# Kernel optimization log

Hardware: AMD Instinct MI355X
Metric: run time of the kernel (lower is better)

## Reference

```python
import jax, jax.numpy as jnp
import numpy as np

B, N, OBJ_D, L, EMB_D, H, NANS, VOCAB = 256, 100, 2048, 14, 300, 1024, 3129, 19901


def gru_last_hidden(x, wih, whh, bih, bhh):
    # x: [B, L, EMB_D]; PyTorch GRU gate order (r, z, n); returns last hidden [B, H]
    h0 = jnp.zeros((x.shape[0], whh.shape[0]), x.dtype)

    def step(h, xt):
        gi = xt @ wih + bih          # [B, 3H]
        gh = h @ whh + bhh           # [B, 3H]
        ir, iz, inn = jnp.split(gi, 3, axis=-1)
        hr, hz, hn = jnp.split(gh, 3, axis=-1)
        r = jax.nn.sigmoid(ir + hr)
        z = jax.nn.sigmoid(iz + hz)
        n = jnp.tanh(inn + r * hn)
        h = (1.0 - z) * n + z * h
        return h, None

    h, _ = jax.lax.scan(step, h0, jnp.swapaxes(x, 0, 1))
    return h


def setup_inputs() -> dict:
    key = jax.random.key(0)
    ks = jax.random.split(key, 24)
    g = lambda k, shp, s: jax.random.normal(k, shp, dtype=jnp.float32) * s
    inp = {
        "v": g(ks[0], (B, N, OBJ_D), 1.0),
        "b": jax.random.uniform(ks[1], (B, N, 6), dtype=jnp.float32),
        "det": jax.random.randint(ks[2], (B, N), 0, 1600),
        "q": jax.random.randint(ks[3], (B, L), 0, VOCAB),
        "labels": jax.random.randint(ks[4], (B,), 0, NANS),
        # word embedding
        "emb": g(ks[5], (VOCAB, EMB_D), 0.02),
        # GRU (input 300 -> hidden 1024)
        "gru_wih": g(ks[6], (EMB_D, 3 * H), 0.02),
        "gru_whh": g(ks[7], (H, 3 * H), 0.02),
        "gru_bih": jnp.zeros((3 * H,), jnp.float32),
        "gru_bhh": jnp.zeros((3 * H,), jnp.float32),
        # q_net FCNet
        "wq_net": g(ks[8], (H, H), 0.02),
        "bq_net": jnp.zeros((H,), jnp.float32),
        # s_rel: spatial relation scorer (uses b[:,:,:4])
        "ws_b": g(ks[9], (4, H), 0.1),
        "ws_q": g(ks[10], (H, H), 0.02),
        # v_rel: visual relation scorer
        "wv_v": g(ks[11], (OBJ_D, H), 0.02),
        "wv_q": g(ks[12], (H, H), 0.02),
        # v_att: NewAttention
        "wa_v": g(ks[13], (OBJ_D, H), 0.02),
        "wa_q": g(ks[14], (H, H), 0.02),
        "wa_out": g(ks[15], (H,), 0.02),
        # v_net FCNet
        "wv_net": g(ks[16], (OBJ_D, H), 0.02),
        "bv_net": jnp.zeros((H,), jnp.float32),
        # classifier MLP 1024 -> 2048 -> 3129
        "wc1": g(ks[17], (H, 2 * H), 0.02),
        "bc1": jnp.zeros((2 * H,), jnp.float32),
        "wc2": g(ks[18], (2 * H, NANS), 0.02),
        "bc2": jnp.zeros((NANS,), jnp.float32),
    }
    return inp


def reference(v, b, det, q, labels, emb, gru_wih, gru_whh, gru_bih, gru_bhh,
              wq_net, bq_net, ws_b, ws_q, wv_v, wv_q, wa_v, wa_q, wa_out,
              wv_net, bv_net, wc1, bc1, wc2, bc2):
    # question encoding
    w_emb = emb[q]                                           # [B, L, 300]
    q_emb = gru_last_hidden(w_emb, gru_wih, gru_whh, gru_bih, gru_bhh)  # [B, H]
    q_repr = jax.nn.relu(q_emb @ wq_net + bq_net)            # [B, H]

    # pairwise relation matrices conditioned on the question
    b4 = b[:, :, :4]                                         # [B, N, 4]
    s_proj = jnp.tanh(b4 @ ws_b)                             # [B, N, H]
    s_q = jnp.tanh(q_emb @ ws_q)                             # [B, H]
    s_rel = jnp.einsum('bnh,bmh->bnm', s_proj * s_q[:, None, :], s_proj)

    v_proj = jnp.tanh(v @ wv_v)                              # [B, N, H]
    v_q = jnp.tanh(q_emb @ wv_q)                             # [B, H]
    v_rel = jnp.einsum('bnh,bmh->bnm', v_proj * v_q[:, None, :], v_proj)

    rel = jax.nn.softmax(s_rel + v_rel, axis=2)              # [B, N, N]
    v_nbr = jnp.einsum('bnm,bmd->bnd', rel, v)               # neighbor aggregation
    v2 = v + v_nbr                                           # [B, N, OBJ_D]

    # attention pooling
    av = jax.nn.relu(v2 @ wa_v)                              # [B, N, H]
    aq = jax.nn.relu(q_emb @ wa_q)                           # [B, H]
    att_logits = (av * aq[:, None, :]) @ wa_out              # [B, N]
    v_att = jax.nn.softmax(att_logits, axis=1)[:, :, None]   # [B, N, 1]
    v_emb = (v_att * v2).sum(axis=1)                         # [B, OBJ_D]

    v_repr = jax.nn.relu(v_emb @ wv_net + bv_net)            # [B, H]
    joint = q_repr * v_repr                                  # [B, H]
    logits = jax.nn.relu(joint @ wc1 + bc1) @ wc2 + bc2      # [B, NANS]
    return logits
```

## Files before the change

kernel.cpp:

```cpp
#include <hip/hip_runtime.h>
#include <math.h>

#define B_    256
#define N_    100
#define OBJD  2048
#define L_    14
#define EMBD  300
#define H_    1024
#define H3    3072
#define NANS_ 3129

typedef unsigned short u16;
typedef unsigned int   u32;
typedef long long      ll;
typedef __attribute__((ext_vector_type(8))) short    s16x8;
typedef __attribute__((ext_vector_type(8))) u16      u16x8;
typedef __attribute__((ext_vector_type(4))) float    f32x4;

__device__ __forceinline__ void split2(float x, u16& h, u16& l) {
    const u32 u = __float_as_uint(x);
    h = (u16)(u >> 16);
    const float r = x - __uint_as_float(u & 0xffff0000u);
    l = (u16)(__float_as_uint(r) >> 16);
}
__device__ __forceinline__ float b2f(u16 v) { return __uint_as_float(((u32)v) << 16); }
__device__ __forceinline__ float tanh_fast(float v) {
    const float e = __expf(2.f * v);
    return 1.f - 2.f * __builtin_amdgcn_rcpf(e + 1.f);
}

template<int BM,int BN,int BK,int TM,int TN,int ACT,int EPI,bool GATHER>
__global__ __launch_bounds__(256)
void gemm_f32(const float* __restrict__ A, long long sA, int lda,
              const float* __restrict__ Bm, long long sB, int ldb,
              const float* __restrict__ bias,
              const float* __restrict__ src, long long sSrc, int ldsrc,
              float* __restrict__ C, u16* __restrict__ Chi, u16* __restrict__ Clo,
              long long sC, int ldc,
              int M, int N, int K, const int* __restrict__ gidx)
{
    static_assert((BM*BK)%1024==0 && (BK*BN)%1024==0 && (BM/TM)*(BN/TN)==256, "cfg");
    constexpr int AV = (BM*BK)/1024, BV = (BK*BN)/1024;
    __shared__ float As[BK][BM+4];
    __shared__ float Bs[BK][BN+4];
    const int bz = blockIdx.z;
    A  += (long long)bz * sA;
    Bm += (long long)bz * sB;
    if (EPI != 3) C += (long long)bz * sC;
    if (EPI) src += (long long)bz * sSrc;
    if constexpr (EPI == 3) { Chi += (long long)bz * sC; Clo += (long long)bz * sC; }

    const int tid = threadIdx.x;
    const int m0 = blockIdx.y * BM, n0 = blockIdx.x * BN;
    const int tx = tid % (BN/TN), ty = tid / (BN/TN);
    const bool bvec = ((ldb & 3) == 0);

    float acc[TM][TN];
#pragma unroll
    for (int i=0;i<TM;i++)
#pragma unroll
      for (int j=0;j<TN;j++) acc[i][j] = 0.f;

    for (int k0 = 0; k0 < K; k0 += BK) {
#pragma unroll
        for (int u=0; u<AV; u++) {
            const int flat = (tid + u*256) * 4;
            const int r = flat / BK, c = flat % BK;
            const int gr = m0 + r, gk = k0 + c;
            float4 a4 = make_float4(0.f,0.f,0.f,0.f);
            if (gr < M) {
                const float* arow = GATHER ? (A + (long long)gidx[gr]*lda)
                                           : (A + (long long)gr*lda);
                if (gk + 3 < K) a4 = *(const float4*)(arow + gk);
                else {
                    float t0[4] = {0.f,0.f,0.f,0.f};
#pragma unroll
                    for (int i=0;i<4;i++) if (gk+i < K) t0[i] = arow[gk+i];
                    a4 = make_float4(t0[0],t0[1],t0[2],t0[3]);
                }
            }
            As[c+0][r]=a4.x; As[c+1][r]=a4.y; As[c+2][r]=a4.z; As[c+3][r]=a4.w;
        }
#pragma unroll
        for (int u=0; u<BV; u++) {
            const int flat = (tid + u*256) * 4;
            const int r = flat / BN, c = flat % BN;
            const int gk = k0 + r, gc = n0 + c;
            float4 b4 = make_float4(0.f,0.f,0.f,0.f);
            if (gk < K) {
                const float* brow = Bm + (long long)gk * ldb;
                if (bvec && (gc + 3 < N)) b4 = *(const float4*)(brow + gc);
                else {
                    float t0[4] = {0.f,0.f,0.f,0.f};
#pragma unroll
                    for (int i=0;i<4;i++) if (gc+i < N) t0[i] = brow[gc+i];
                    b4 = make_float4(t0[0],t0[1],t0[2],t0[3]);
                }
            }
            Bs[r][c+0]=b4.x; Bs[r][c+1]=b4.y; Bs[r][c+2]=b4.z; Bs[r][c+3]=b4.w;
        }
        __syncthreads();
#pragma unroll
        for (int kk=0;kk<BK;kk++) {
            float a[TM], b[TN];
#pragma unroll
            for (int p=0;p<TM/4;p++) {
                float4 t4 = *(const float4*)&As[kk][ty*TM + 4*p];
                a[4*p]=t4.x; a[4*p+1]=t4.y; a[4*p+2]=t4.z; a[4*p+3]=t4.w;
            }
#pragma unroll
            for (int p=0;p<TN/4;p++) {
                float4 t4 = *(const float4*)&Bs[kk][tx*TN + 4*p];
                b[4*p]=t4.x; b[4*p+1]=t4.y; b[4*p+2]=t4.z; b[4*p+3]=t4.w;
            }
#pragma unroll
            for (int i=0;i<TM;i++)
#pragma unroll
                for (int j=0;j<TN;j++) acc[i][j] = fmaf(a[i], b[j], acc[i][j]);
        }
        __syncthreads();
    }
#pragma unroll
    for (int i=0;i<TM;i++) {
        const int r = m0 + ty*TM + i;
        if (r >= M) continue;
#pragma unroll
        for (int j=0;j<TN;j++) {
            const int c = n0 + tx*TN + j;
            if (c >= N) continue;
            float val = acc[i][j];
            if (bias) val += bias[c];
            if (EPI == 1 || EPI == 3) val += src[(long long)r*ldsrc + c];
            if constexpr (EPI == 3) {
                u16 h, l; split2(val, h, l);
                Chi[(long long)r*ldc + c] = h;
                Clo[(long long)r*ldc + c] = l;
            } else {
                C[(long long)r*ldc + c] = val;
            }
        }
    }
}

__global__ __launch_bounds__(256)
void split_transpose_w(const float* __restrict__ W, u16* __restrict__ Thi,
                       u16* __restrict__ Tlo, int Kin, int Nin, int Kld)
{
    __shared__ float tile[64][33];
    const int k0 = blockIdx.x*64, n0 = blockIdx.y*32;
    const int t = threadIdx.x;
    const int ln = t & 31, lk = t >> 5;
#pragma unroll
    for (int i=0;i<8;i++) {
        const int k = k0 + lk + i*8, n = n0 + ln;
        tile[lk + i*8][ln] = (k < Kin && n < Nin) ? W[(long long)k*Nin + n] : 0.f;
    }
    __syncthreads();
    const int wn = t >> 3, wk = (t & 7) * 8;
    u16x8 hv, lv;
#pragma unroll
    for (int i=0;i<8;i++){
        u16 h, l; split2(tile[wk + i][wn], h, l);
        hv[i] = h; lv[i] = l;
    }
    *(u16x8*)&Thi[(long long)(n0+wn)*Kld + k0 + wk] = hv;
    *(u16x8*)&Tlo[(long long)(n0+wn)*Kld + k0 + wk] = lv;
}

__global__ __launch_bounds__(256)
void split_rows(const float* __restrict__ x, u16* __restrict__ hi,
                u16* __restrict__ lo, long long n8)
{
    for (long long i = blockIdx.x*256 + threadIdx.x; i < n8; i += (long long)gridDim.x*256) {
        const float4 a = ((const float4*)x)[2*i];
        const float4 c = ((const float4*)x)[2*i+1];
        const float f[8] = {a.x,a.y,a.z,a.w,c.x,c.y,c.z,c.w};
        u16x8 h, l;
#pragma unroll
        for (int e=0;e<8;e++){ u16 hh,ll_; split2(f[e],hh,ll_); h[e]=hh; l[e]=ll_; }
        ((u16x8*)hi)[i] = h;
        ((u16x8*)lo)[i] = l;
    }
}

template<int BM, int ACT, int EPI, bool BIAS>
__global__ __launch_bounds__(256, (BM==256)?2:3)
void gemm3s(const u16* __restrict__ Ahi, const u16* __restrict__ Alo, int lda,
            const u16* __restrict__ BThi, const u16* __restrict__ BTlo,
            const float* __restrict__ bias,
            const float* __restrict__ src, int ldsrc,
            float* __restrict__ C, u16* __restrict__ Chi, u16* __restrict__ Clo,
            int ldc, int N, int K)
{
    constexpr int BN=128, BK=32, PK=40;
    constexpr int MF = BM/32;
    __shared__ __align__(16) u16 smem[2*BM*PK + 2*BN*PK];
    u16* Ah = smem;
    u16* Al = smem + BM*PK;
    u16* Bh = smem + 2*BM*PK;
    u16* Bl = Bh + BN*PK;

    const int tid = threadIdx.x;
    const int m0 = blockIdx.y*BM, n0 = blockIdx.x*BN;
    const int wave = tid>>6, lane = tid&63;
    const int wm = wave>>1, wn = wave&1;
    const int r16 = lane&15, g = lane>>4;

    f32x4 acc[MF][4];
#pragma unroll
    for (int i=0;i<MF;i++)
#pragma unroll
      for (int j=0;j<4;j++) acc[i][j] = f32x4{0.f,0.f,0.f,0.f};

    const int ar = (BM==256) ? tid : (tid>>2);
    const int ac = (BM==256) ? 0   : ((tid&3)*8);
    const u16* pAh = Ahi + (long long)(m0+ar)*lda + ac;
    const u16* pAl = Alo + (long long)(m0+ar)*lda + ac;
    u16* sAh = Ah + ar*PK + ac;
    u16* sAl = Al + ar*PK + ac;
    const int br = tid>>1, bc = (tid&1)*16;
    const u16* pBh = BThi + (long long)(n0+br)*K + bc;
    const u16* pBl = BTlo + (long long)(n0+br)*K + bc;
    u16* sBh = Bh + br*PK + bc;
    u16* sBl = Bl + br*PK + bc;

    for (int k0=0; k0<K; k0+=BK) {
        __syncthreads();
        if constexpr (BM==256) {
#pragma unroll
            for (int u=0;u<4;u++){
                *(u16x8*)(sAh+u*8) = *(const u16x8*)(pAh + k0 + u*8);
                *(u16x8*)(sAl+u*8) = *(const u16x8*)(pAl + k0 + u*8);
            }
        } else {
            *(u16x8*)sAh = *(const u16x8*)(pAh + k0);
            *(u16x8*)sAl = *(const u16x8*)(pAl + k0);
        }
        *(u16x8*)(sBh)   = *(const u16x8*)(pBh + k0);
        *(u16x8*)(sBh+8) = *(const u16x8*)(pBh + k0 + 8);
        *(u16x8*)(sBl)   = *(const u16x8*)(pBl + k0);
        *(u16x8*)(sBl+8) = *(const u16x8*)(pBl + k0 + 8);
        __syncthreads();

        s16x8 bh[4], bl[4];
#pragma unroll
        for (int nf=0;nf<4;nf++){
            bh[nf] = *(const s16x8*)&Bh[(wn*64 + nf*16 + r16)*PK + g*8];
            bl[nf] = *(const s16x8*)&Bl[(wn*64 + nf*16 + r16)*PK + g*8];
        }
#pragma unroll
        for (int mf=0; mf<MF; mf++){
            const s16x8 ah = *(const s16x8*)&Ah[(wm*(BM/2) + mf*16 + r16)*PK + g*8];
            const s16x8 al = *(const s16x8*)&Al[(wm*(BM/2) + mf*16 + r16)*PK + g*8];
#pragma unroll
            for (int nf=0;nf<4;nf++){
                acc[mf][nf] = __builtin_amdgcn_mfma_f32_16x16x32_bf16(ah, bh[nf], acc[mf][nf], 0,0,0);
                acc[mf][nf] = __builtin_amdgcn_mfma_f32_16x16x32_bf16(ah, bl[nf], acc[mf][nf], 0,0,0);
                acc[mf][nf] = __builtin_amdgcn_mfma_f32_16x16x32_bf16(al, bh[nf], acc[mf][nf], 0,0,0);
            }
        }
    }
#pragma unroll
    for (int mf=0;mf<MF;mf++){
        const int rr = m0 + wm*(BM/2) + mf*16 + g*4;
#pragma unroll
        for (int nf=0;nf<4;nf++){
            const int cc = n0 + wn*64 + nf*16 + r16;
            if (cc >= N) continue;
            const float bval = BIAS ? bias[cc] : 0.f;
#pragma unroll
            for (int i=0;i<4;i++){
                float val = acc[mf][nf][i] + bval;
                if (ACT == 1) val = fmaxf(val, 0.f);
                else if (ACT == 2) val = tanh_fast(val);
                else if (ACT == 3) {
                    const int seg = cc >> 10;
                    val = (seg==0 || seg==3) ? fmaxf(val, 0.f) : tanh_fast(val);
                }
                if (EPI == 2) val *= src[(long long)(rr+i)*ldsrc + cc];
                const long long o = (long long)(rr+i)*ldc + cc;
                C[o] = val;
                if (EPI >= 1) {
                    u16 h, l; split2(val, h, l);
                    Chi[o] = h; Clo[o] = l;
                }
            }
        }
    }
}

__global__ __launch_bounds__(192)
void gru_step(const float* __restrict__ hprev,
              const u16* __restrict__ hHi, const u16* __restrict__ hLo,
              const u16* __restrict__ whhThi, const u16* __restrict__ whhTlo,
              const float* __restrict__ gi, int t, const float* __restrict__ bhh,
              float* __restrict__ hout, u16* __restrict__ hoHi, u16* __restrict__ hoLo)
{
    constexpr int PK = 40;
    __shared__ __align__(16) u16 smem[8*32*PK];
    u16* Ah = smem;
    u16* Al = smem + 32*PK;
    const int tid = threadIdx.x, seg = tid>>6, lane = tid&63;
    u16* Bh = smem + 2*32*PK + seg*2*32*PK;
    u16* Bl = Bh + 32*PK;
    const int j0 = blockIdx.x*32, b0 = blockIdx.y*32;
    const int r16 = lane&15, g = lane>>4;
    f32x4 acc[2][2];
#pragma unroll
    for (int i=0;i<2;i++)
#pragma unroll
      for (int j=0;j<2;j++) acc[i][j] = f32x4{0.f,0.f,0.f,0.f};

    const int sr = lane>>1, sc = (lane&1)*16;
    const u16* pAh = hHi + (long long)(b0+sr)*H_ + sc;
    const u16* pAl = hLo + (long long)(b0+sr)*H_ + sc;
    const u16* pBh = whhThi + (long long)(seg*H_ + j0 + sr)*H_ + sc;
    const u16* pBl = whhTlo + (long long)(seg*H_ + j0 + sr)*H_ + sc;
    u16* sAh = Ah + sr*PK + sc;
    u16* sAl = Al + sr*PK + sc;
    u16* sBh = Bh + sr*PK + sc;
    u16* sBl = Bl + sr*PK + sc;

    for (int k0=0; k0<H_; k0+=32) {
        __syncthreads();
        if (seg == 0) {
            *(u16x8*)(sAh)   = *(const u16x8*)(pAh + k0);
            *(u16x8*)(sAh+8) = *(const u16x8*)(pAh + k0 + 8);
            *(u16x8*)(sAl)   = *(const u16x8*)(pAl + k0);
            *(u16x8*)(sAl+8) = *(const u16x8*)(pAl + k0 + 8);
        }
        *(u16x8*)(sBh)   = *(const u16x8*)(pBh + k0);
        *(u16x8*)(sBh+8) = *(const u16x8*)(pBh + k0 + 8);
        *(u16x8*)(sBl)   = *(const u16x8*)(pBl + k0);
        *(u16x8*)(sBl+8) = *(const u16x8*)(pBl + k0 + 8);
        __syncthreads();
        s16x8 bh[2], bl[2];
#pragma unroll
        for (int nf=0;nf<2;nf++){
            bh[nf] = *(const s16x8*)&Bh[(nf*16 + r16)*PK + g*8];
            bl[nf] = *(const s16x8*)&Bl[(nf*16 + r16)*PK + g*8];
        }
#pragma unroll
        for (int mf=0;mf<2;mf++){
            const s16x8 ah = *(const s16x8*)&Ah[(mf*16 + r16)*PK + g*8];
            const s16x8 al = *(const s16x8*)&Al[(mf*16 + r16)*PK + g*8];
#pragma unroll
            for (int nf=0;nf<2;nf++){
                acc[mf][nf] = __builtin_amdgcn_mfma_f32_16x16x32_bf16(ah, bh[nf], acc[mf][nf], 0,0,0);
                acc[mf][nf] = __builtin_amdgcn_mfma_f32_16x16x32_bf16(ah, bl[nf], acc[mf][nf], 0,0,0);
                acc[mf][nf] = __builtin_amdgcn_mfma_f32_16x16x32_bf16(al, bh[nf], acc[mf][nf], 0,0,0);
            }
        }
    }
    __syncthreads();
    float* ghb = (float*)smem;
#pragma unroll
    for (int mf=0;mf<2;mf++)
#pragma unroll
      for (int nf=0;nf<2;nf++)
#pragma unroll
        for (int i=0;i<4;i++)
            ghb[(seg*32 + mf*16 + g*4 + i)*32 + nf*16 + r16] = acc[mf][nf][i];
    __syncthreads();
    for (int idx = tid; idx < 1024; idx += 192) {
        const int r = idx>>5, c = idx&31;
        const int b = b0 + r, j = j0 + c;
        const float* gib = gi + ((long long)b*L_ + t)*H3 + j;
        const float ir = gib[0], iz = gib[H_], inn = gib[2*H_];
        const float hr = ghb[(0*32+r)*32+c] + bhh[j];
        const float hz = ghb[(1*32+r)*32+c] + bhh[j+H_];
        const float hn = ghb[(2*32+r)*32+c] + bhh[j+2*H_];
        const float hp = hprev[(long long)b*H_ + j];
        const float rg = 1.f/(1.f+expf(-(ir+hr)));
        const float zg = 1.f/(1.f+expf(-(iz+hz)));
        const float nn = tanhf(inn + rg*hn);
        const float ho = (1.f - zg)*nn + zg*hp;
        hout[(long long)b*H_ + j] = ho;
        u16 hh, hl; split2(ho, hh, hl);
        hoHi[(long long)b*H_ + j] = hh;
        hoLo[(long long)b*H_ + j] = hl;
    }
}

__global__ __launch_bounds__(256)
void gru_t0(const float* __restrict__ gi, const float* __restrict__ bhh,
            float* __restrict__ h, u16* __restrict__ hHi, u16* __restrict__ hLo)
{
    const int idx = blockIdx.x*256 + threadIdx.x;
    const int b = idx >> 10, j = idx & (H_-1);
    const float* gib = gi + ((long long)b*L_)*H3 + j;
    const float ir = gib[0], iz = gib[H_], inn = gib[2*H_];
    const float rg = 1.f/(1.f+expf(-(ir+bhh[j])));
    const float zg = 1.f/(1.f+expf(-(iz+bhh[j+H_])));
    const float nn = tanhf(inn + rg*bhh[j+2*H_]);
    const float ho = (1.f - zg)*nn;
    h[idx] = ho;
    u16 hh, hl; split2(ho, hh, hl);
    hHi[idx] = hh; hLo[idx] = hl;
}

__global__ __launch_bounds__(256)
void build_qbias(const float* __restrict__ bq, float* __restrict__ qb)
{
    const int i = blockIdx.x*256 + threadIdx.x;
    if (i < 4096) qb[i] = (i < 1024) ? bq[i] : 0.f;
}

__global__ __launch_bounds__(256)
void sproj_kernel(const float* __restrict__ bIn, const float* __restrict__ wsB,
                  float* __restrict__ sProj)
{
    const int row = blockIdx.x;
    const float* br = bIn + (long long)row * 6;
    const float b0=br[0], b1=br[1], b2=br[2], b3=br[3];
    for (int h = threadIdx.x; h < H_; h += 256) {
        float val = b0*wsB[h] + b1*wsB[H_+h] + b2*wsB[2*H_+h] + b3*wsB[3*H_+h];
        sProj[(long long)row*H_ + h] = tanhf(val);
    }
}

__global__ __launch_bounds__(256)
void gram_rel_kernel(const float* __restrict__ sProj, const float* __restrict__ sQ,
                     const float* __restrict__ vProj, const float* __restrict__ vQ,
                     int ldq, float* __restrict__ rel)
{
    __shared__ float As[16][68];
    __shared__ float Bs[16][68];
    const int b = blockIdx.z;
    const int n0 = blockIdx.y * 64, m0 = blockIdx.x * 64;
    const int tid = threadIdx.x;
    const int lr = tid / 4, lk = (tid % 4) * 4;
    const int tx = tid % 16, ty = tid / 16;
    float acc[4][4];
#pragma unroll
    for (int i=0;i<4;i++)
#pragma unroll
      for (int j=0;j<4;j++) acc[i][j]=0.f;

    for (int pass=0; pass<2; ++pass) {
        const float* P  = pass ? vProj : sProj;
        const float* Q  = (pass ? vQ : sQ) + (long long)b * ldq;
        const float* Pb = P + (long long)b * N_ * H_;
        for (int k0=0; k0<H_; k0+=16) {
            const float4 qv = *(const float4*)(Q + k0 + lk);
            float4 a4 = make_float4(0,0,0,0), b4 = make_float4(0,0,0,0);
            if (n0 + lr < N_) a4 = *(const float4*)(Pb + (long long)(n0+lr)*H_ + k0 + lk);
            if (m0 + lr < N_) b4 = *(const float4*)(Pb + (long long)(m0+lr)*H_ + k0 + lk);
            As[lk+0][lr]=a4.x*qv.x; As[lk+1][lr]=a4.y*qv.y; As[lk+2][lr]=a4.z*qv.z; As[lk+3][lr]=a4.w*qv.w;
            Bs[lk+0][lr]=b4.x; Bs[lk+1][lr]=b4.y; Bs[lk+2][lr]=b4.z; Bs[lk+3][lr]=b4.w;
            __syncthreads();
#pragma unroll
// ... 28 lines not shown
    float* r = rel + ((long long)blockIdx.x*4 + w)*N_;
    const float v0 = r[l];
    const float v1 = (l + 64 < N_) ? r[l+64] : -INFINITY;
    float mx = fmaxf(v0, v1);
    for (int s=32;s;s>>=1) mx = fmaxf(mx, __shfl_xor(mx, s));
    const float e0 = expf(v0-mx);
    const float e1 = (l+64<N_) ? expf(v1-mx) : 0.f;
    float sum = e0+e1;
    for (int s=32;s;s>>=1) sum += __shfl_xor(sum, s);
    const float inv = 1.f/sum;
    r[l] = e0*inv;
    if (l+64 < N_) r[l+64] = e1*inv;
}

__global__ __launch_bounds__(256)
void att_logits_kernel(const float* __restrict__ av, const float* __restrict__ aq,
                       int ldq, const float* __restrict__ waOut, float* __restrict__ out)
{
    const int w = threadIdx.x >> 6, l = threadIdx.x & 63;
    const int row = blockIdx.x*4 + w;
    const int b = row / N_;
    const float* avr = av + (long long)row*H_;
    const float* aqr = aq + (long long)b*ldq;
    float acc = 0.f;
#pragma unroll
    for (int i=0;i<4;i++){
        const int h = i*256 + l*4;
        const float4 a4 = *(const float4*)(avr+h);
        const float4 q4 = *(const float4*)(aqr+h);
        const float4 w4 = *(const float4*)(waOut+h);
        acc += a4.x*q4.x*w4.x + a4.y*q4.y*w4.y + a4.z*q4.z*w4.z + a4.w*q4.w*w4.w;
    }
    for (int s=32;s;s>>=1) acc += __shfl_xor(acc, s);
    if (l==0) out[row] = acc;
}

__global__ __launch_bounds__(128)
void softmax_n_kernel(const float* __restrict__ lg, float* __restrict__ att)
{
    __shared__ float s[128];
    const int b = blockIdx.x, t = threadIdx.x;
    const float v = (t < N_) ? lg[(long long)b*N_+t] : -INFINITY;
    s[t]=v; __syncthreads();
    for (int st=64;st;st>>=1){ if (t<st) s[t]=fmaxf(s[t],s[t+st]); __syncthreads(); }
    const float mx = s[0]; __syncthreads();
    const float e = (t<N_)? expf(v-mx) : 0.f;
    s[t]=e; __syncthreads();
    for (int st=64;st;st>>=1){ if (t<st) s[t]+=s[t+st]; __syncthreads(); }
    const float inv = 1.f/s[0];
    if (t<N_) att[(long long)b*N_+t] = e*inv;
}

__global__ __launch_bounds__(256)
void vemb_kernel(const float* __restrict__ att, const u16* __restrict__ v2hi,
                 const u16* __restrict__ v2lo, u16* __restrict__ veHi,
                 u16* __restrict__ veLo)
{
    __shared__ float sa[N_];
    const int b = blockIdx.y, dt = blockIdx.x, tid = threadIdx.x;
    if (tid < N_) sa[tid] = att[(long long)b*N_+tid];
    __syncthreads();
    const int d = dt*256 + tid;
    const long long base = (long long)b*N_*OBJD + d;
    float acc = 0.f;
#pragma unroll 4
    for (int n=0;n<N_;n++) {
        const long long o = base + (long long)n*OBJD;
        acc += sa[n]*(b2f(v2hi[o]) + b2f(v2lo[o]));
    }
    u16 h, l; split2(acc, h, l);
    veHi[(long long)b*OBJD + d] = h;
    veLo[(long long)b*OBJD + d] = l;
}

extern "C" void kernel_launch(void* const* d_in, const int* in_sizes, int n_in,
                              void* d_out, int out_size, void* d_ws, size_t ws_size,
                              hipStream_t stream)
{
    const float* v      = (const float*)d_in[0];
    const float* bbox   = (const float*)d_in[1];
    const int*   q      = (const int*)  d_in[3];
    const float* emb    = (const float*)d_in[5];
    const float* wih    = (const float*)d_in[6];
    const float* whh    = (const float*)d_in[7];
    const float* bih    = (const float*)d_in[8];
    const float* bhh    = (const float*)d_in[9];
    const float* wq_net = (const float*)d_in[10];
    const float* bq_net = (const float*)d_in[11];
    const float* ws_b   = (const float*)d_in[12];
    const float* ws_q   = (const float*)d_in[13];
    const float* wv_v   = (const float*)d_in[14];
    const float* wv_q   = (const float*)d_in[15];
    const float* wa_v   = (const float*)d_in[16];
    const float* wa_q   = (const float*)d_in[17];
    const float* wa_out = (const float*)d_in[18];
    const float* wv_net = (const float*)d_in[19];
    const float* bv_net = (const float*)d_in[20];
    const float* wc1    = (const float*)d_in[21];
    const float* bc1    = (const float*)d_in[22];
    const float* wc2    = (const float*)d_in[23];
    const float* bc2    = (const float*)d_in[24];
    float* out = (float*)d_out;
    (void)in_sizes; (void)n_in; (void)out_size; (void)ws_size; (void)bih;

    float* ws = (float*)d_ws;
    size_t off = 0;
    auto alloc = [&](size_t n){ float* p = ws + off; off += (n + 63) & ~(size_t)63; return p; };
    float* gi    = alloc((size_t)B_*L_*H3);
    float* h_a   = alloc((size_t)B_*H_);
    float* h_b   = alloc((size_t)B_*H_);
    u16* hhi_a = (u16*)alloc((size_t)B_*H_/2);
    u16* hlo_a = (u16*)alloc((size_t)B_*H_/2);
    u16* hhi_b = (u16*)alloc((size_t)B_*H_/2);
    u16* hlo_b = (u16*)alloc((size_t)B_*H_/2);
    float* qcat  = alloc((size_t)B_*4096);
    float* qbias = alloc(4096);
    float* sproj = alloc((size_t)B_*N_*H_);
    float* vproj = alloc((size_t)B_*N_*H_);
    float* relb  = alloc((size_t)B_*N_*N_);
    u16* vhi = (u16*)alloc((size_t)B_*N_*OBJD/2);
    u16* vlo = (u16*)alloc((size_t)B_*N_*OBJD/2);
    float* avb   = sproj;
    float* attl  = alloc((size_t)B_*N_);
    float* vatt  = alloc((size_t)B_*N_);
    u16* vembHi = (u16*)alloc((size_t)B_*OBJD/2);
    u16* vembLo = (u16*)alloc((size_t)B_*OBJD/2);
    float* jointf = alloc((size_t)B_*H_);
    u16* jointHi = (u16*)alloc((size_t)B_*H_/2);
    u16* jointLo = (u16*)alloc((size_t)B_*H_/2);
    float* c1f   = alloc((size_t)B_*2*H_);
    u16* c1Hi = (u16*)alloc((size_t)B_*H_);
    u16* c1Lo = (u16*)alloc((size_t)B_*H_);
    u16* whhThi = (u16*)alloc((size_t)H3*H_/2);
    u16* whhTlo = (u16*)alloc((size_t)H3*H_/2);
    u16* qcThi  = (u16*)alloc((size_t)4096*H_/2);
    u16* qcTlo  = (u16*)alloc((size_t)4096*H_/2);
    u16* wvvThi = (u16*)alloc((size_t)H_*OBJD/2);
    u16* wvvTlo = (u16*)alloc((size_t)H_*OBJD/2);
    u16* wavThi = (u16*)alloc((size_t)H_*OBJD/2);
    u16* wavTlo = (u16*)alloc((size_t)H_*OBJD/2);
    u16* wvnThi = (u16*)alloc((size_t)H_*OBJD/2);
    u16* wvnTlo = (u16*)alloc((size_t)H_*OBJD/2);
    u16* wc1Thi = (u16*)alloc((size_t)2*H_*H_/2);
    u16* wc1Tlo = (u16*)alloc((size_t)2*H_*H_/2);
    u16* wc2Thi = (u16*)alloc((size_t)3200*2*H_/2);
    u16* wc2Tlo = (u16*)alloc((size_t)3200*2*H_/2);

    split_transpose_w<<<dim3(H_/64, H3/32),256,0,stream>>>(whh, whhThi, whhTlo, H_, H3, H_);
    split_transpose_w<<<dim3(H_/64, H_/32),256,0,stream>>>(wq_net, qcThi + (size_t)0*H_*H_, qcTlo + (size_t)0*H_*H_, H_, H_, H_);
    split_transpose_w<<<dim3(H_/64, H_/32),256,0,stream>>>(ws_q,   qcThi + (size_t)1*H_*H_, qcTlo + (size_t)1*H_*H_, H_, H_, H_);
    split_transpose_w<<<dim3(H_/64, H_/32),256,0,stream>>>(wv_q,   qcThi + (size_t)2*H_*H_, qcTlo + (size_t)2*H_*H_, H_, H_, H_);
    split_transpose_w<<<dim3(H_/64, H_/32),256,0,stream>>>(wa_q,   qcThi + (size_t)3*H_*H_, qcTlo + (size_t)3*H_*H_, H_, H_, H_);
    split_transpose_w<<<dim3(OBJD/64, H_/32),256,0,stream>>>(wv_v, wvvThi, wvvTlo, OBJD, H_, OBJD);
    split_transpose_w<<<dim3(OBJD/64, H_/32),256,0,stream>>>(wa_v, wavThi, wavTlo, OBJD, H_, OBJD);
    split_transpose_w<<<dim3(OBJD/64, H_/32),256,0,stream>>>(wv_net, wvnThi, wvnTlo, OBJD, H_, OBJD);
    split_transpose_w<<<dim3(H_/64, 2*H_/32),256,0,stream>>>(wc1, wc1Thi, wc1Tlo, H_, 2*H_, H_);
    split_transpose_w<<<dim3(2*H_/64, 3200/32),256,0,stream>>>(wc2, wc2Thi, wc2Tlo, 2*H_, NANS_, 2*H_);
    split_rows<<<2048,256,0,stream>>>(v, vhi, vlo, (long long)B_*N_*OBJD/8);
    build_qbias<<<16,256,0,stream>>>(bq_net, qbias);

    {
        dim3 g(H3/128, (B_*L_+127)/128, 1);
        gemm_f32<128,128,16,8,8,0,0,true><<<g,256,0,stream>>>(
            emb,0,EMBD, wih,0,H3, bih, nullptr,0,0, gi,nullptr,nullptr,0,H3, B_*L_, H3, EMBD, q);
    }
    gru_t0<<<(B_*H_)/256,256,0,stream>>>(gi, bhh, h_a, hhi_a, hlo_a);
    float* hp = h_a; u16* hpHi = hhi_a; u16* hpLo = hlo_a;
    float* hn = h_b; u16* hnHi = hhi_b; u16* hnLo = hlo_b;
    for (int t=1;t<L_;t++){
        gru_step<<<dim3(H_/32, B_/32),192,0,stream>>>(hp, hpHi, hpLo, whhThi, whhTlo,
                                                      gi, t, bhh, hn, hnHi, hnLo);
        float* tf=hp; hp=hn; hn=tf;
        u16* th=hpHi; hpHi=hnHi; hnHi=th;
        u16* tl=hpLo; hpLo=hnLo; hnLo=tl;
    }
    gemm3s<64,3,0,true><<<dim3(4096/128, B_/64),256,0,stream>>>(
        hpHi, hpLo, H_, qcThi, qcTlo, qbias, nullptr,0,
        qcat, nullptr, nullptr, 4096, 4096, H_);
    const float* qrepr = qcat;
    const float* sq    = qcat + 1024;
    const float* vq    = qcat + 2048;
    const float* aq    = qcat + 3072;

    sproj_kernel<<<B_*N_,256,0,stream>>>(bbox, ws_b, sproj);
    gemm3s<256,2,0,false><<<dim3(H_/128, (B_*N_)/256),256,0,stream>>>(
        vhi, vlo, OBJD, wvvThi, wvvTlo, nullptr, nullptr,0,
        vproj, nullptr, nullptr, H_, H_, OBJD);
    gram_rel_kernel<<<dim3(2,2,B_),256,0,stream>>>(sproj, sq, vproj, vq, 4096, relb);
    softmax_m_kernel<<<(B_*N_)/4,256,0,stream>>>(relb);
    {
        dim3 g(OBJD/64, (N_+63)/64, B_);
        gemm_f32<64,64,16,4,4,0,3,false><<<g,256,0,stream>>>(
            relb,(long long)N_*N_,N_, v,(long long)N_*OBJD,OBJD, nullptr,
            v,(long long)N_*OBJD,OBJD, nullptr, vhi, vlo,
            (long long)N_*OBJD, OBJD, N_, OBJD, N_, nullptr);
    }
    gemm3s<256,1,0,false><<<dim3(H_/128, (B_*N_)/256),256,0,stream>>>(
        vhi, vlo, OBJD, wavThi, wavTlo, nullptr, nullptr,0,
        avb, nullptr, nullptr, H_, H_, OBJD);
    att_logits_kernel<<<(B_*N_)/4,256,0,stream>>>(avb, aq, 4096, wa_out, attl);
    softmax_n_kernel<<<B_,128,0,stream>>>(attl, vatt);
    vemb_kernel<<<dim3(OBJD/256,B_),256,0,stream>>>(vatt, vhi, vlo, vembHi, vembLo);
    gemm3s<64,1,2,true><<<dim3(H_/128, B_/64),256,0,stream>>>(
        vembHi, vembLo, OBJD, wvnThi, wvnTlo, bv_net, qrepr, 4096,
        jointf, jointHi, jointLo, H_, H_, OBJD);
    gemm3s<64,1,1,true><<<dim3(2*H_/128, B_/64),256,0,stream>>>(
        jointHi, jointLo, H_, wc1Thi, wc1Tlo, bc1, nullptr,0,
        c1f, c1Hi, c1Lo, 2*H_, 2*H_, H_);
    gemm3s<64,0,0,true><<<dim3(3200/128, B_/64),256,0,stream>>>(
        c1Hi, c1Lo, 2*H_, wc2Thi, wc2Tlo, bc2, nullptr,0,
        out, nullptr, nullptr, NANS_, NANS_, 2*H_);
}
```

Before: 2.986 ms.

## Interleave hi/lo bf16 splits per 32-column chunk and retile big GEMMs

Activation hi/lo bf16 halves are now stored interleaved in 32-element chunks within one buffer, so each K-step load fetches both halves from one contiguous 128-byte region. The large v-projection GEMMs move from 256-row tiles to a 128x128 kernel with register prefetch of the next K tile and an XCD-aware block-to-tile mapping meant to improve L2 reuse of A rows. The small GEMMs get a dedicated 64-row kernel with the new layout. The risks are lower occupancy from the extra prefetch registers and more scattered 16-bit stores in the epilogues that write the split.

```diff
diff --git a/kernel.cpp b/kernel.cpp
--- a/kernel.cpp
+++ b/kernel.cpp
@@ -12,7 +12,6 @@
 
 typedef unsigned short u16;
 typedef unsigned int   u32;
-typedef long long      ll;
 typedef __attribute__((ext_vector_type(8))) short    s16x8;
 typedef __attribute__((ext_vector_type(8))) u16      u16x8;
 typedef __attribute__((ext_vector_type(4))) float    f32x4;
@@ -29,13 +28,13 @@
     return 1.f - 2.f * __builtin_amdgcn_rcpf(e + 1.f);
 }
 
-template<int BM,int BN,int BK,int TM,int TN,int ACT,int EPI,bool GATHER>
+template<int BM,int BN,int BK,int TM,int TN,int EPI,bool GATHER>
 __global__ __launch_bounds__(256)
 void gemm_f32(const float* __restrict__ A, long long sA, int lda,
               const float* __restrict__ Bm, long long sB, int ldb,
               const float* __restrict__ bias,
               const float* __restrict__ src, long long sSrc, int ldsrc,
-              float* __restrict__ C, u16* __restrict__ Chi, u16* __restrict__ Clo,
+              float* __restrict__ C, u16* __restrict__ Csp,
               long long sC, int ldc,
               int M, int N, int K, const int* __restrict__ gidx)
 {
@@ -48,7 +47,7 @@
     Bm += (long long)bz * sB;
     if (EPI != 3) C += (long long)bz * sC;
     if (EPI) src += (long long)bz * sSrc;
-    if constexpr (EPI == 3) { Chi += (long long)bz * sC; Clo += (long long)bz * sC; }
+    if constexpr (EPI == 3) Csp += (long long)bz * sC * 2;
 
     const int tid = threadIdx.x;
     const int m0 = blockIdx.y * BM, n0 = blockIdx.x * BN;
@@ -130,11 +129,11 @@
             if (c >= N) continue;
             float val = acc[i][j];
             if (bias) val += bias[c];
-            if (EPI == 1 || EPI == 3) val += src[(long long)r*ldsrc + c];
+            if (EPI == 3) val += src[(long long)r*ldsrc + c];
             if constexpr (EPI == 3) {
                 u16 h, l; split2(val, h, l);
-                Chi[(long long)r*ldc + c] = h;
-                Clo[(long long)r*ldc + c] = l;
+                const long long os = (long long)r*2*ldc + ((c>>5)<<6) + (c&31);
+                Csp[os] = h; Csp[os+32] = l;
             } else {
                 C[(long long)r*ldc + c] = val;
             }
@@ -168,101 +167,179 @@
 }
 
 __global__ __launch_bounds__(256)
-void split_rows(const float* __restrict__ x, u16* __restrict__ hi,
-                u16* __restrict__ lo, long long n8)
-{
-    for (long long i = blockIdx.x*256 + threadIdx.x; i < n8; i += (long long)gridDim.x*256) {
-        const float4 a = ((const float4*)x)[2*i];
-        const float4 c = ((const float4*)x)[2*i+1];
-        const float f[8] = {a.x,a.y,a.z,a.w,c.x,c.y,c.z,c.w};
-        u16x8 h, l;
-#pragma unroll
-        for (int e=0;e<8;e++){ u16 hh,ll_; split2(f[e],hh,ll_); h[e]=hh; l[e]=ll_; }
-        ((u16x8*)hi)[i] = h;
-        ((u16x8*)lo)[i] = l;
-    }
-}
-
-template<int BM, int ACT, int EPI, bool BIAS>
-__global__ __launch_bounds__(256, (BM==256)?2:3)
-void gemm3s(const u16* __restrict__ Ahi, const u16* __restrict__ Alo, int lda,
-            const u16* __restrict__ BThi, const u16* __restrict__ BTlo,
-            const float* __restrict__ bias,
-            const float* __restrict__ src, int ldsrc,
-            float* __restrict__ C, u16* __restrict__ Chi, u16* __restrict__ Clo,
-            int ldc, int N, int K)
-{
-    constexpr int BN=128, BK=32, PK=40;
-    constexpr int MF = BM/32;
-    __shared__ __align__(16) u16 smem[2*BM*PK + 2*BN*PK];
-    u16* Ah = smem;
-    u16* Al = smem + BM*PK;
-    u16* Bh = smem + 2*BM*PK;
-    u16* Bl = Bh + BN*PK;
+void split_rows_il(const float* __restrict__ x, u16* __restrict__ sp, long long ngran)
+{
+    for (long long g = blockIdx.x*256 + threadIdx.x; g < ngran; g += (long long)gridDim.x*256) {
+        const float4* s4 = (const float4*)(x + g*32);
+        u16* o = sp + g*64;
+        u16x8 hv[4], lv[4];
+#pragma unroll
+        for (int q=0;q<4;q++){
+            const float4 f0 = s4[2*q], f1 = s4[2*q+1];
+            const float fa[8]={f0.x,f0.y,f0.z,f0.w,f1.x,f1.y,f1.z,f1.w};
+#pragma unroll
+            for (int e=0;e<8;e++){ u16 hh,ll2; split2(fa[e],hh,ll2); hv[q][e]=hh; lv[q][e]=ll2; }
+        }
+#pragma unroll
+        for (int q=0;q<4;q++){ *(u16x8*)(o+q*8)=hv[q]; *(u16x8*)(o+32+q*8)=lv[q]; }
+    }
+}
+
+template<int ACT>
+__global__ __launch_bounds__(256, 3)
+void gemm3s128(const u16* __restrict__ Asp, int lda2,
+               const u16* __restrict__ BThi, const u16* __restrict__ BTlo,
+               float* __restrict__ C, int ldc, int N, int K, int rpx)
+{
+    constexpr int PK=40;
+    __shared__ __align__(16) u16 Ah[128*PK];
+    __shared__ __align__(16) u16 Al[128*PK];
+    __shared__ __align__(16) u16 Bh[128*PK];
+    __shared__ __align__(16) u16 Bl[128*PK];
+
+    const int wgid = blockIdx.x;
+    const int xcd  = wgid & 7;
+    const int j    = wgid >> 3;
+    const int m0   = (xcd*rpx + (j>>3)) * 128;
+    const int n0   = (j & 7) * 128;
 
     const int tid = threadIdx.x;
-    const int m0 = blockIdx.y*BM, n0 = blockIdx.x*BN;
     const int wave = tid>>6, lane = tid&63;
     const int wm = wave>>1, wn = wave&1;
     const int r16 = lane&15, g = lane>>4;
 
-    f32x4 acc[MF][4];
-#pragma unroll
-    for (int i=0;i<MF;i++)
-#pragma unroll
-      for (int j=0;j<4;j++) acc[i][j] = f32x4{0.f,0.f,0.f,0.f};
-
-    const int ar = (BM==256) ? tid : (tid>>2);
-    const int ac = (BM==256) ? 0   : ((tid&3)*8);
-    const u16* pAh = Ahi + (long long)(m0+ar)*lda + ac;
-    const u16* pAl = Alo + (long long)(m0+ar)*lda + ac;
-    u16* sAh = Ah + ar*PK + ac;
-    u16* sAl = Al + ar*PK + ac;
-    const int br = tid>>1, bc = (tid&1)*16;
-    const u16* pBh = BThi + (long long)(n0+br)*K + bc;
-    const u16* pBl = BTlo + (long long)(n0+br)*K + bc;
-    u16* sBh = Bh + br*PK + bc;
-    u16* sBl = Bl + br*PK + bc;
-
-    for (int k0=0; k0<K; k0+=BK) {
+    f32x4 acc[4][4];
+#pragma unroll
+    for (int i=0;i<4;i++)
+#pragma unroll
+      for (int jj=0;jj<4;jj++) acc[i][jj] = f32x4{0.f,0.f,0.f,0.f};
+
+    const int r = tid>>1, half = tid&1;
+    const u16* pA = Asp + (long long)(m0+r)*lda2 + half*32;
+    const u16* pB = (half ? BTlo : BThi) + (long long)(n0+r)*K;
+    u16* sA = (half ? Al : Ah) + r*PK;
+    u16* sB = (half ? Bl : Bh) + r*PK;
+
+    u16x8 ra0,ra1,ra2,ra3, rb0,rb1,rb2,rb3;
+    {
+        ra0=*(const u16x8*)pA;      ra1=*(const u16x8*)(pA+8);
+        ra2=*(const u16x8*)(pA+16); ra3=*(const u16x8*)(pA+24);
+        rb0=*(const u16x8*)pB;      rb1=*(const u16x8*)(pB+8);
+        rb2=*(const u16x8*)(pB+16); rb3=*(const u16x8*)(pB+24);
+    }
+    for (int k0=0; k0<K; k0+=32) {
         __syncthreads();
-        if constexpr (BM==256) {
-#pragma unroll
-            for (int u=0;u<4;u++){
-                *(u16x8*)(sAh+u*8) = *(const u16x8*)(pAh + k0 + u*8);
-                *(u16x8*)(sAl+u*8) = *(const u16x8*)(pAl + k0 + u*8);
-            }
-        } else {
-            *(u16x8*)sAh = *(const u16x8*)(pAh + k0);
-            *(u16x8*)sAl = *(const u16x8*)(pAl + k0);
-        }
-        *(u16x8*)(sBh)   = *(const u16x8*)(pBh + k0);
-        *(u16x8*)(sBh+8) = *(const u16x8*)(pBh + k0 + 8);
-        *(u16x8*)(sBl)   = *(const u16x8*)(pBl + k0);
-        *(u16x8*)(sBl+8) = *(const u16x8*)(pBl + k0 + 8);
+        *(u16x8*)(sA)=ra0; *(u16x8*)(sA+8)=ra1; *(u16x8*)(sA+16)=ra2; *(u16x8*)(sA+24)=ra3;
+        *(u16x8*)(sB)=rb0; *(u16x8*)(sB+8)=rb1; *(u16x8*)(sB+16)=rb2; *(u16x8*)(sB+24)=rb3;
+        if (k0+32 < K) {
+            const u16* a = pA + (long long)(k0+32)*2;
+            const u16* b = pB + (k0+32);
+            ra0=*(const u16x8*)a;      ra1=*(const u16x8*)(a+8);
+            ra2=*(const u16x8*)(a+16); ra3=*(const u16x8*)(a+24);
+            rb0=*(const u16x8*)b;      rb1=*(const u16x8*)(b+8);
+            rb2=*(const u16x8*)(b+16); rb3=*(const u16x8*)(b+24);
+        }
         __syncthreads();
-
-        s16x8 bh[4], bl[4];
+        s16x8 bhf[4], blf[4];
 #pragma unroll
         for (int nf=0;nf<4;nf++){
-            bh[nf] = *(const s16x8*)&Bh[(wn*64 + nf*16 + r16)*PK + g*8];
-            bl[nf] = *(const s16x8*)&Bl[(wn*64 + nf*16 + r16)*PK + g*8];
-        }
-#pragma unroll
-        for (int mf=0; mf<MF; mf++){
-            const s16x8 ah = *(const s16x8*)&Ah[(wm*(BM/2) + mf*16 + r16)*PK + g*8];
-            const s16x8 al = *(const s16x8*)&Al[(wm*(BM/2) + mf*16 + r16)*PK + g*8];
+            bhf[nf] = *(const s16x8*)&Bh[(wn*64 + nf*16 + r16)*PK + g*8];
+            blf[nf] = *(const s16x8*)&Bl[(wn*64 + nf*16 + r16)*PK + g*8];
+        }
+#pragma unroll
+        for (int mf=0;mf<4;mf++){
+            const s16x8 ah = *(const s16x8*)&Ah[(wm*64 + mf*16 + r16)*PK + g*8];
+            const s16x8 al = *(const s16x8*)&Al[(wm*64 + mf*16 + r16)*PK + g*8];
 #pragma unroll
             for (int nf=0;nf<4;nf++){
-                acc[mf][nf] = __builtin_amdgcn_mfma_f32_16x16x32_bf16(ah, bh[nf], acc[mf][nf], 0,0,0);
-                acc[mf][nf] = __builtin_amdgcn_mfma_f32_16x16x32_bf16(ah, bl[nf], acc[mf][nf], 0,0,0);
-                acc[mf][nf] = __builtin_amdgcn_mfma_f32_16x16x32_bf16(al, bh[nf], acc[mf][nf], 0,0,0);
-            }
-        }
-    }
-#pragma unroll
-    for (int mf=0;mf<MF;mf++){
-        const int rr = m0 + wm*(BM/2) + mf*16 + g*4;
+                acc[mf][nf] = __builtin_amdgcn_mfma_f32_16x16x32_bf16(ah, bhf[nf], acc[mf][nf],0,0,0);
+                acc[mf][nf] = __builtin_amdgcn_mfma_f32_16x16x32_bf16(ah, blf[nf], acc[mf][nf],0,0,0);
+                acc[mf][nf] = __builtin_amdgcn_mfma_f32_16x16x32_bf16(al, bhf[nf], acc[mf][nf],0,0,0);
+            }
+        }
+    }
+#pragma unroll
+    for (int mf=0;mf<4;mf++){
+        const int rr = m0 + wm*64 + mf*16 + g*4;
+#pragma unroll
+        for (int nf=0;nf<4;nf++){
+            const int cc = n0 + wn*64 + nf*16 + r16;
+            if (cc >= N) continue;
+#pragma unroll
+            for (int i=0;i<4;i++){
+                float val = acc[mf][nf][i];
+                if (ACT==1) val = fmaxf(val,0.f);
+                else if (ACT==2) val = tanh_fast(val);
+                C[(long long)(rr+i)*ldc + cc] = val;
+            }
+        }
+    }
+}
+
+template<int ACT, int EPI, bool BIAS>
+__global__ __launch_bounds__(256, 3)
+void gemm3s64(const u16* __restrict__ Asp, int lda2,
+              const u16* __restrict__ BThi, const u16* __restrict__ BTlo,
+              const float* __restrict__ bias,
+              const float* __restrict__ src, int ldsrc,
+              float* __restrict__ C, u16* __restrict__ Csp,
+              int ldc, int N, int K)
+{
+    constexpr int PK=40;
+    __shared__ __align__(16) u16 Ah[64*PK];
+    __shared__ __align__(16) u16 Al[64*PK];
+    __shared__ __align__(16) u16 Bh[128*PK];
+    __shared__ __align__(16) u16 Bl[128*PK];
+
+    const int tid = threadIdx.x;
+    const int m0 = blockIdx.y*64, n0 = blockIdx.x*128;
+    const int wave = tid>>6, lane = tid&63;
+    const int wm = wave>>1, wn = wave&1;
+    const int r16 = lane&15, g = lane>>4;
+
+    f32x4 acc[2][4];
+#pragma unroll
+    for (int i=0;i<2;i++)
+#pragma unroll
+      for (int jj=0;jj<4;jj++) acc[i][jj] = f32x4{0.f,0.f,0.f,0.f};
+
+    const int ar = tid>>2, aq = tid&3;
+    const u16* pA = Asp + (long long)(m0+ar)*lda2 + aq*16;
+    u16* sA = ((aq<2) ? Ah : Al) + ar*PK + (aq&1)*16;
+    const int rb = tid>>1, hb = tid&1;
+    const u16* pB = (hb ? BTlo : BThi) + (long long)(n0+rb)*K;
+    u16* sB = (hb ? Bl : Bh) + rb*PK;
+
+    for (int k0=0; k0<K; k0+=32) {
+        __syncthreads();
+        *(u16x8*)(sA)   = *(const u16x8*)(pA + (long long)k0*2);
+        *(u16x8*)(sA+8) = *(const u16x8*)(pA + (long long)k0*2 + 8);
+        *(u16x8*)(sB)    = *(const u16x8*)(pB + k0);
+        *(u16x8*)(sB+8)  = *(const u16x8*)(pB + k0 + 8);
+        *(u16x8*)(sB+16) = *(const u16x8*)(pB + k0 + 16);
+        *(u16x8*)(sB+24) = *(const u16x8*)(pB + k0 + 24);
+        __syncthreads();
+        s16x8 bhf[4], blf[4];
+#pragma unroll
+        for (int nf=0;nf<4;nf++){
+            bhf[nf] = *(const s16x8*)&Bh[(wn*64 + nf*16 + r16)*PK + g*8];
+            blf[nf] = *(const s16x8*)&Bl[(wn*64 + nf*16 + r16)*PK + g*8];
+        }
+#pragma unroll
+        for (int mf=0;mf<2;mf++){
+            const s16x8 ah = *(const s16x8*)&Ah[(wm*32 + mf*16 + r16)*PK + g*8];
+            const s16x8 al = *(const s16x8*)&Al[(wm*32 + mf*16 + r16)*PK + g*8];
+#pragma unroll
+            for (int nf=0;nf<4;nf++){
+                acc[mf][nf] = __builtin_amdgcn_mfma_f32_16x16x32_bf16(ah, bhf[nf], acc[mf][nf],0,0,0);
+                acc[mf][nf] = __builtin_amdgcn_mfma_f32_16x16x32_bf16(ah, blf[nf], acc[mf][nf],0,0,0);
+                acc[mf][nf] = __builtin_amdgcn_mfma_f32_16x16x32_bf16(al, bhf[nf], acc[mf][nf],0,0,0);
+            }
+        }
+    }
+#pragma unroll
+    for (int mf=0;mf<2;mf++){
+        const int rr = m0 + wm*32 + mf*16 + g*4;
 #pragma unroll
         for (int nf=0;nf<4;nf++){
             const int cc = n0 + wn*64 + nf*16 + r16;
@@ -278,11 +355,11 @@
                     val = (seg==0 || seg==3) ? fmaxf(val, 0.f) : tanh_fast(val);
                 }
                 if (EPI == 2) val *= src[(long long)(rr+i)*ldsrc + cc];
-                const long long o = (long long)(rr+i)*ldc + cc;
-                C[o] = val;
+                C[(long long)(rr+i)*ldc + cc] = val;
                 if (EPI >= 1) {
                     u16 h, l; split2(val, h, l);
-                    Chi[o] = h; Clo[o] = l;
+                    const long long os = (long long)(rr+i)*2*ldc + ((cc>>5)<<6) + (cc&31);
+                    Csp[os] = h; Csp[os+32] = l;
                 }
             }
         }
@@ -290,11 +367,10 @@
 }
 
 __global__ __launch_bounds__(192)
-void gru_step(const float* __restrict__ hprev,
-              const u16* __restrict__ hHi, const u16* __restrict__ hLo,
+void gru_step(const float* __restrict__ hprev, const u16* __restrict__ hsp,
               const u16* __restrict__ whhThi, const u16* __restrict__ whhTlo,
               const float* __restrict__ gi, int t, const float* __restrict__ bhh,
-              float* __restrict__ hout, u16* __restrict__ hoHi, u16* __restrict__ hoLo)
+              float* __restrict__ hout, u16* __restrict__ hosp)
 {
     constexpr int PK = 40;
     __shared__ __align__(16) u16 smem[8*32*PK];
@@ -311,23 +387,23 @@
 #pragma unroll
       for (int j=0;j<2;j++) acc[i][j] = f32x4{0.f,0.f,0.f,0.f};
 
+    const int rA = lane>>1, hA = lane&1;
+    const u16* pA = hsp + (long long)(b0+rA)*(2*H_) + hA*32;
+    u16* sA = (hA ? Al : Ah) + rA*PK;
     const int sr = lane>>1, sc = (lane&1)*16;
-    const u16* pAh = hHi + (long long)(b0+sr)*H_ + sc;
-    const u16* pAl = hLo + (long long)(b0+sr)*H_ + sc;
     const u16* pBh = whhThi + (long long)(seg*H_ + j0 + sr)*H_ + sc;
     const u16* pBl = whhTlo + (long long)(seg*H_ + j0 + sr)*H_ + sc;
-    u16* sAh = Ah + sr*PK + sc;
-    u16* sAl = Al + sr*PK + sc;
     u16* sBh = Bh + sr*PK + sc;
     u16* sBl = Bl + sr*PK + sc;
 
     for (int k0=0; k0<H_; k0+=32) {
         __syncthreads();
         if (seg == 0) {
-            *(u16x8*)(sAh)   = *(const u16x8*)(pAh + k0);
-            *(u16x8*)(sAh+8) = *(const u16x8*)(pAh + k0 + 8);
-            *(u16x8*)(sAl)   = *(const u16x8*)(pAl + k0);
-            *(u16x8*)(sAl+8) = *(const u16x8*)(pAl + k0 + 8);
+            const u16* a = pA + (long long)k0*2;
+            *(u16x8*)(sA)    = *(const u16x8*)(a);
+            *(u16x8*)(sA+8)  = *(const u16x8*)(a+8);
+            *(u16x8*)(sA+16) = *(const u16x8*)(a+16);
+            *(u16x8*)(sA+24) = *(const u16x8*)(a+24);
         }
         *(u16x8*)(sBh)   = *(const u16x8*)(pBh + k0);
         *(u16x8*)(sBh+8) = *(const u16x8*)(pBh + k0 + 8);
@@ -377,14 +453,14 @@
         const float ho = (1.f - zg)*nn + zg*hp;
         hout[(long long)b*H_ + j] = ho;
         u16 hh, hl; split2(ho, hh, hl);
-        hoHi[(long long)b*H_ + j] = hh;
-        hoLo[(long long)b*H_ + j] = hl;
+        const long long ob = (long long)b*(2*H_) + ((j>>5)<<6) + (j&31);
+        hosp[ob] = hh; hosp[ob+32] = hl;
     }
 }
 
 __global__ __launch_bounds__(256)
 void gru_t0(const float* __restrict__ gi, const float* __restrict__ bhh,
-            float* __restrict__ h, u16* __restrict__ hHi, u16* __restrict__ hLo)
+            float* __restrict__ h, u16* __restrict__ hsp)
 {
     const int idx = blockIdx.x*256 + threadIdx.x;
     const int b = idx >> 10, j = idx & (H_-1);
@@ -396,7 +472,8 @@
     const float ho = (1.f - zg)*nn;
     h[idx] = ho;
     u16 hh, hl; split2(ho, hh, hl);
-    hHi[idx] = hh; hLo[idx] = hl;
+    const long long ob = (long long)b*(2*H_) + ((j>>5)<<6) + (j&31);
+    hsp[ob] = hh; hsp[ob+32] = hl;
 }
 
 __global__ __launch_bounds__(256)
@@ -531,25 +608,25 @@
 }
 
 __global__ __launch_bounds__(256)
-void vemb_kernel(const float* __restrict__ att, const u16* __restrict__ v2hi,
-                 const u16* __restrict__ v2lo, u16* __restrict__ veHi,
-                 u16* __restrict__ veLo)
+void vemb_kernel(const float* __restrict__ att, const u16* __restrict__ v2sp,
+                 u16* __restrict__ vesp)
 {
     __shared__ float sa[N_];
     const int b = blockIdx.y, dt = blockIdx.x, tid = threadIdx.x;
     if (tid < N_) sa[tid] = att[(long long)b*N_+tid];
     __syncthreads();
     const int d = dt*256 + tid;
-    const long long base = (long long)b*N_*OBJD + d;
+    const long long colo = (long long)((d>>5)<<6) + (d&31);
+    const u16* vb = v2sp + (long long)b*N_*(2*OBJD) + colo;
     float acc = 0.f;
 #pragma unroll 4
     for (int n=0;n<N_;n++) {
-        const long long o = base + (long long)n*OBJD;
-        acc += sa[n]*(b2f(v2hi[o]) + b2f(v2lo[o]));
+        const u16* p = vb + (long long)n*(2*OBJD);
+        acc += sa[n]*(b2f(p[0]) + b2f(p[32]));
     }
     u16 h, l; split2(acc, h, l);
-    veHi[(long long)b*OBJD + d] = h;
-    veLo[(long long)b*OBJD + d] = l;
+    const long long o = (long long)b*(2*OBJD) + colo;
+    vesp[o] = h; vesp[o+32] = l;
 }
 
 extern "C" void kernel_launch(void* const* d_in, const int* in_sizes, int n_in,
@@ -588,28 +665,22 @@
     float* gi    = alloc((size_t)B_*L_*H3);
     float* h_a   = alloc((size_t)B_*H_);
     float* h_b   = alloc((size_t)B_*H_);
-    u16* hhi_a = (u16*)alloc((size_t)B_*H_/2);
-    u16* hlo_a = (u16*)alloc((size_t)B_*H_/2);
-    u16* hhi_b = (u16*)alloc((size_t)B_*H_/2);
-    u16* hlo_b = (u16*)alloc((size_t)B_*H_/2);
+    u16* hsp_a = (u16*)alloc((size_t)B_*H_);
+    u16* hsp_b = (u16*)alloc((size_t)B_*H_);
     float* qcat  = alloc((size_t)B_*4096);
     float* qbias = alloc(4096);
     float* sproj = alloc((size_t)B_*N_*H_);
     float* vproj = alloc((size_t)B_*N_*H_);
     float* relb  = alloc((size_t)B_*N_*N_);
-    u16* vhi = (u16*)alloc((size_t)B_*N_*OBJD/2);
-    u16* vlo = (u16*)alloc((size_t)B_*N_*OBJD/2);
+    u16* vsp  = (u16*)alloc((size_t)B_*N_*OBJD);
     float* avb   = sproj;
     float* attl  = alloc((size_t)B_*N_);
     float* vatt  = alloc((size_t)B_*N_);
-    u16* vembHi = (u16*)alloc((size_t)B_*OBJD/2);
-    u16* vembLo = (u16*)alloc((size_t)B_*OBJD/2);
+    u16* vembsp = (u16*)alloc((size_t)B_*OBJD);
     float* jointf = alloc((size_t)B_*H_);
-    u16* jointHi = (u16*)alloc((size_t)B_*H_/2);
-    u16* jointLo = (u16*)alloc((size_t)B_*H_/2);
+    u16* jointsp = (u16*)alloc((size_t)B_*H_);
     float* c1f   = alloc((size_t)B_*2*H_);
-    u16* c1Hi = (u16*)alloc((size_t)B_*H_);
-    u16* c1Lo = (u16*)alloc((size_t)B_*H_);
+    u16* c1sp = (u16*)alloc((size_t)B_*2*H_);
     u16* whhThi = (u16*)alloc((size_t)H3*H_/2);
     u16* whhTlo = (u16*)alloc((size_t)H3*H_/2);
     u16* qcThi  = (u16*)alloc((size_t)4096*H_/2);
@@ -635,58 +706,55 @@
     split_transpose_w<<<dim3(OBJD/64, H_/32),256,0,stream>>>(wv_net, wvnThi, wvnTlo, OBJD, H_, OBJD);
     split_transpose_w<<<dim3(H_/64, 2*H_/32),256,0,stream>>>(wc1, wc1Thi, wc1Tlo, H_, 2*H_, H_);
     split_transpose_w<<<dim3(2*H_/64, 3200/32),256,0,stream>>>(wc2, wc2Thi, wc2Tlo, 2*H_, NANS_, 2*H_);
-    split_rows<<<2048,256,0,stream>>>(v, vhi, vlo, (long long)B_*N_*OBJD/8);
+    split_rows_il<<<2048,256,0,stream>>>(v, vsp, (long long)B_*N_*OBJD/32);
     build_qbias<<<16,256,0,stream>>>(bq_net, qbias);
 
     {
         dim3 g(H3/128, (B_*L_+127)/128, 1);
-        gemm_f32<128,128,16,8,8,0,0,true><<<g,256,0,stream>>>(
-            emb,0,EMBD, wih,0,H3, bih, nullptr,0,0, gi,nullptr,nullptr,0,H3, B_*L_, H3, EMBD, q);
-    }
-    gru_t0<<<(B_*H_)/256,256,0,stream>>>(gi, bhh, h_a, hhi_a, hlo_a);
-    float* hp = h_a; u16* hpHi = hhi_a; u16* hpLo = hlo_a;
-    float* hn = h_b; u16* hnHi = hhi_b; u16* hnLo = hlo_b;
+        gemm_f32<128,128,16,8,8,0,true><<<g,256,0,stream>>>(
+            emb,0,EMBD, wih,0,H3, bih, nullptr,0,0, gi,nullptr,0,H3, B_*L_, H3, EMBD, q);
+    }
+    gru_t0<<<(B_*H_)/256,256,0,stream>>>(gi, bhh, h_a, hsp_a);
+    float* hp = h_a; u16* hpS = hsp_a;
+    float* hn = h_b; u16* hnS = hsp_b;
     for (int t=1;t<L_;t++){
-        gru_step<<<dim3(H_/32, B_/32),192,0,stream>>>(hp, hpHi, hpLo, whhThi, whhTlo,
-                                                      gi, t, bhh, hn, hnHi, hnLo);
+        gru_step<<<dim3(H_/32, B_/32),192,0,stream>>>(hp, hpS, whhThi, whhTlo,
+                                                      gi, t, bhh, hn, hnS);
         float* tf=hp; hp=hn; hn=tf;
-        u16* th=hpHi; hpHi=hnHi; hnHi=th;
-        u16* tl=hpLo; hpLo=hnLo; hnLo=tl;
-    }
-    gemm3s<64,3,0,true><<<dim3(4096/128, B_/64),256,0,stream>>>(
-        hpHi, hpLo, H_, qcThi, qcTlo, qbias, nullptr,0,
-        qcat, nullptr, nullptr, 4096, 4096, H_);
+        u16* th=hpS; hpS=hnS; hnS=th;
+    }
+    gemm3s64<3,0,true><<<dim3(4096/128, B_/64),256,0,stream>>>(
+        hpS, 2*H_, qcThi, qcTlo, qbias, nullptr,0,
+        qcat, nullptr, 4096, 4096, H_);
     const float* qrepr = qcat;
     const float* sq    = qcat + 1024;
     const float* vq    = qcat + 2048;
     const float* aq    = qcat + 3072;
 
     sproj_kernel<<<B_*N_,256,0,stream>>>(bbox, ws_b, sproj);
-    gemm3s<256,2,0,false><<<dim3(H_/128, (B_*N_)/256),256,0,stream>>>(
-        vhi, vlo, OBJD, wvvThi, wvvTlo, nullptr, nullptr,0,
-        vproj, nullptr, nullptr, H_, H_, OBJD);
+    gemm3s128<2><<<(B_*N_/128)*8,256,0,stream>>>(
+        vsp, 2*OBJD, wvvThi, wvvTlo, vproj, H_, H_, OBJD, (B_*N_/128)/8);
     gram_rel_kernel<<<dim3(2,2,B_),256,0,stream>>>(sproj, sq, vproj, vq, 4096, relb);
     softmax_m_kernel<<<(B_*N_)/4,256,0,stream>>>(relb);
     {
         dim3 g(OBJD/64, (N_+63)/64, B_);
-        gemm_f32<64,64,16,4,4,0,3,false><<<g,256,0,stream>>>(
+        gemm_f32<64,64,16,4,4,3,false><<<g,256,0,stream>>>(
             relb,(long long)N_*N_,N_, v,(long long)N_*OBJD,OBJD, nullptr,
-            v,(long long)N_*OBJD,OBJD, nullptr, vhi, vlo,
+            v,(long long)N_*OBJD,OBJD, nullptr, vsp,
             (long long)N_*OBJD, OBJD, N_, OBJD, N_, nullptr);
     }
-    gemm3s<256,1,0,false><<<dim3(H_/128, (B_*N_)/256),256,0,stream>>>(
-        vhi, vlo, OBJD, wavThi, wavTlo, nullptr, nullptr,0,
-        avb, nullptr, nullptr, H_, H_, OBJD);
+    gemm3s128<1><<<(B_*N_/128)*8,256,0,stream>>>(
+        vsp, 2*OBJD, wavThi, wavTlo, avb, H_, H_, OBJD, (B_*N_/128)/8);
     att_logits_kernel<<<(B_*N_)/4,256,0,stream>>>(avb, aq, 4096, wa_out, attl);
     softmax_n_kernel<<<B_,128,0,stream>>>(attl, vatt);
-    vemb_kernel<<<dim3(OBJD/256,B_),256,0,stream>>>(vatt, vhi, vlo, vembHi, vembLo);
-    gemm3s<64,1,2,true><<<dim3(H_/128, B_/64),256,0,stream>>>(
-        vembHi, vembLo, OBJD, wvnThi, wvnTlo, bv_net, qrepr, 4096,
-        jointf, jointHi, jointLo, H_, H_, OBJD);
-    gemm3s<64,1,1,true><<<dim3(2*H_/128, B_/64),256,0,stream>>>(
-        jointHi, jointLo, H_, wc1Thi, wc1Tlo, bc1, nullptr,0,
-        c1f, c1Hi, c1Lo, 2*H_, 2*H_, H_);
-    gemm3s<64,0,0,true><<<dim3(3200/128, B_/64),256,0,stream>>>(
-        c1Hi, c1Lo, 2*H_, wc2Thi, wc2Tlo, bc2, nullptr,0,
-        out, nullptr, nullptr, NANS_, NANS_, 2*H_);
-}
+    vemb_kernel<<<dim3(OBJD/256,B_),256,0,stream>>>(vatt, vsp, vembsp);
+    gemm3s64<1,2,true><<<dim3(H_/128, B_/64),256,0,stream>>>(
+        vembsp, 2*OBJD, wvnThi, wvnTlo, bv_net, qrepr, 4096,
+        jointf, jointsp, H_, H_, OBJD);
+    gemm3s64<1,1,true><<<dim3(2*H_/128, B_/64),256,0,stream>>>(
+        jointsp, 2*H_, wc1Thi, wc1Tlo, bc1, nullptr,0,
+        c1f, c1sp, 2*H_, 2*H_, H_);
+    gemm3s64<0,0,true><<<dim3(3200/128, B_/64),256,0,stream>>>(
+        c1sp, 2*2*H_, wc2Thi, wc2Tlo, bc2, nullptr,0,
+        out, nullptr, NANS_, NANS_, 2*H_);
+}
```

Result: faster. 2.691 ms (-9.9%).
